# Kernel tuning notes

Hardware: AMD Instinct MI355X
Metric: run time of the kernel (lower is better)

The kernel has to match this reference:

```python
import jax, jax.numpy as jnp
import numpy as np

B, T, C, H = 4, 4096, 512, 64  # batch, seq(patches), n_embed, head_size

def setup_inputs() -> dict:
    key = jax.random.key(0)
    kx, kk, kq, kv = jax.random.split(key, 4)
    x = jax.random.normal(kx, (B, T, C), dtype=jnp.float32)
    # torch nn.Linear(n_embed, head_size).weight is [H, C]; store transposed [C, H]
    Wk = jax.random.normal(kk, (C, H), dtype=jnp.float32) / np.sqrt(C)
    Wq = jax.random.normal(kq, (C, H), dtype=jnp.float32) / np.sqrt(C)
    Wv = jax.random.normal(kv, (C, H), dtype=jnp.float32) / np.sqrt(C)
    return {"x": x, "Wk": Wk, "Wq": Wq, "Wv": Wv}

def reference(x, Wk, Wq, Wv):
    Bn, Tn, Cn = x.shape
    k = x @ Wk  # [B,T,H]
    q = x @ Wq
    v = x @ Wv
    # NOTE: original scales by C**-0.5 with C = n_embed (input dim), not head_size
    scores = jnp.einsum('bth,bsh->bts', q, k) * (Cn ** -0.5)  # [B,T,T]
    causal = jnp.tril(jnp.ones((Tn, Tn), dtype=bool))
    scores = jnp.where(causal, scores, -jnp.inf)
    attn = jax.nn.softmax(scores, axis=-1)
    return jnp.einsum('bts,bsh->bth', attn, v)  # [B,T,H]
```

## Files before the change

### kernel.cpp

```cpp
#include <hip/hip_runtime.h>
#include <hip/hip_bf16.h>

#define Bb 4
#define Tt 4096

typedef __bf16 bf16;
typedef __attribute__((ext_vector_type(8))) __bf16 bf16x8;
typedef __attribute__((ext_vector_type(4))) __bf16 bf16x4;
typedef __attribute__((ext_vector_type(2))) __bf16 bf16x2;
typedef __attribute__((ext_vector_type(4))) float f32x4;
typedef __attribute__((ext_vector_type(2))) unsigned int u32x2;
typedef __attribute__((ext_vector_type(4))) unsigned int u32x4;


__global__ __launch_bounds__(256) void wt_kernel(const float* __restrict__ Wk,
                                                 const float* __restrict__ Wq,
                                                 const float* __restrict__ Wv,
                                                 bf16* __restrict__ wt) {
  int idx = blockIdx.x * 256 + threadIdx.x;
  int mat = idx >> 15;
  int rem = idx & 32767;
  int n = rem >> 9;
  int k = rem & 511;
  const float* W = (mat == 0) ? Wk : (mat == 1) ? Wq : Wv;
  float v = W[k * 64 + n];
  if (mat == 1) v *= 0.0637587165f;
  wt[idx] = (bf16)v;
}

__global__ __launch_bounds__(256) void proj_kernel(const float* __restrict__ x,
                                                   const bf16* __restrict__ wt,
                                                   bf16* __restrict__ Kb,
                                                   bf16* __restrict__ Qb,
                                                   bf16* __restrict__ VTb) {
  __shared__ __attribute__((aligned(16))) bf16 xs[16][520];
  int tid = threadIdx.x;
  int row0 = blockIdx.x * 16;

  int sr = tid >> 4, sc = (tid & 15) * 4;
  const float* xr = x + (size_t)(row0 + sr) * 512;
#pragma unroll
  for (int j = 0; j < 8; ++j) {
    f32x4 a = *(const f32x4*)(xr + sc + j * 64);
    bf16x4 h;
#pragma unroll
    for (int e = 0; e < 4; ++e) h[e] = (bf16)a[e];
    *(bf16x4*)&xs[sr][sc + j * 64] = h;
  }
  __syncthreads();

  int wave = tid >> 6, lane = tid & 63, m = lane & 15, quad = lane >> 4;
  f32x4 acc[3];
#pragma unroll
  for (int i = 0; i < 3; ++i) acc[i] = (f32x4){0.f, 0.f, 0.f, 0.f};

#pragma unroll 4
  for (int kk = 0; kk < 512; kk += 32) {
    bf16x8 af = *(const bf16x8*)&xs[m][kk + quad * 8];
#pragma unroll
    for (int i = 0; i < 3; ++i) {
      int nt = wave * 3 + i;
      bf16x8 bfr = *(const bf16x8*)(wt + (nt >> 2) * 32768 +
                                    (((nt & 3) * 16) + m) * 512 + kk + quad * 8);
      acc[i] = __builtin_amdgcn_mfma_f32_16x16x32_bf16(af, bfr, acc[i], 0, 0, 0);
    }
  }

  int b = row0 >> 12, tloc = row0 & 4095;
#pragma unroll
  for (int i = 0; i < 3; ++i) {
    int nt = wave * 3 + i, mat = nt >> 2, n0 = (nt & 3) * 16;
    if (mat == 2) {
      bf16x4 pv;
#pragma unroll
      for (int r = 0; r < 4; ++r) pv[r] = (bf16)acc[i][r];
      *(bf16x4*)&VTb[((size_t)b * 64 + n0 + m) * 4096 + tloc + quad * 4] = pv;
    } else {
      bf16* dst = (mat == 0) ? Kb : Qb;
#pragma unroll
      for (int r = 0; r < 4; ++r)
        dst[(size_t)(row0 + quad * 4 + r) * 64 + n0 + m] = (bf16)acc[i][r];
    }
  }
}

static __device__ inline unsigned pk2(float lo, float hi) {
  bf16x2 t;
  t[0] = (bf16)lo;
  t[1] = (bf16)hi;
  return __builtin_bit_cast(unsigned int, t);
}
static __device__ inline void plswap(unsigned& a, unsigned& b) {
  u32x2 r = __builtin_amdgcn_permlane16_swap(a, b, false, false);
  a = r.x;
  b = r.y;
}

__global__ __launch_bounds__(256, 3) void attn_kernel(const bf16* __restrict__ Qb,
                                                      const bf16* __restrict__ Kb,
                                                      const bf16* __restrict__ VTb,
                                                      bf16* __restrict__ Opart,
                                                      float* __restrict__ Lpart,
                                                      float* __restrict__ out) {
  __shared__ __attribute__((aligned(16))) bf16 Kt[2][64][72];
  __shared__ __attribute__((aligned(16))) bf16 Vt[2][64][72];

  int tid = threadIdx.x, wave = tid >> 6, lane = tid & 63;
  int m = lane & 15, quad = lane >> 4, kq = quad * 8;

  int uu = 575 - (int)blockIdx.x;
  int b = uu / 144, u2 = uu % 144;
  int g = 0;
  while (u2 >= 2 * (g + 1) * (g + 2)) ++g;
  int rr = u2 - 2 * g * (g + 1);
  int qi2 = 4 * g + rr / (g + 1);
  int c = rr % (g + 1);
  int t0 = qi2 * 128;
  int s_beg = c * 512;
  int s_end = min(s_beg + 512, t0 + 128);
  int niter = (s_end - s_beg) >> 6;

  const bf16* Qp = Qb + ((size_t)b * Tt + t0 + wave * 16 + m) * 64;
  bf16x8 aq00 = *(const bf16x8*)(Qp + kq);
  bf16x8 aq01 = *(const bf16x8*)(Qp + 32 + kq);
  bf16x8 aq10 = *(const bf16x8*)(Qp + 4096 + kq);
  bf16x8 aq11 = *(const bf16x8*)(Qp + 4096 + 32 + kq);

  bf16x8 onesb;
#pragma unroll
  for (int j = 0; j < 8; ++j) onesb[j] = (bf16)1.0f;

  f32x4 o0[4], o1[4];
#pragma unroll
  for (int i = 0; i < 4; ++i) {
    o0[i] = (f32x4){0.f, 0.f, 0.f, 0.f};
    o1[i] = (f32x4){0.f, 0.f, 0.f, 0.f};
  }
  f32x4 lsum0 = (f32x4){0.f, 0.f, 0.f, 0.f};
  f32x4 lsum1 = (f32x4){0.f, 0.f, 0.f, 0.f};

  int r_ = tid >> 2, seg = tid & 3;
  const bf16* Kbase = Kb + (size_t)b * Tt * 64;
  const bf16* VTbase = VTb + (size_t)b * 64 * 4096;

  {
    const bf16* ks = Kbase + (size_t)(s_beg + r_) * 64 + seg * 16;
    bf16x8 k0 = *(const bf16x8*)ks;
    bf16x8 k1 = *(const bf16x8*)(ks + 8);
    const bf16* vs = VTbase + (size_t)r_ * 4096 + s_beg + seg * 16;
    bf16x8 v0 = *(const bf16x8*)vs;
    bf16x8 v1 = *(const bf16x8*)(vs + 8);
    *(bf16x8*)&Kt[0][r_][seg * 16] = k0;
    *(bf16x8*)&Kt[0][r_][seg * 16 + 8] = k1;
    *(bf16x8*)&Vt[0][r_][seg * 16] = v0;
    *(bf16x8*)&Vt[0][r_][seg * 16 + 8] = v1;
  }
  __syncthreads();

  int qrow0 = t0 + wave * 16 + m;

  for (int i = 0; i < niter; ++i) {
    int kv0 = s_beg + i * 64;
    int cb = i & 1;
    bool more = (i + 1 < niter);

    bf16x8 k0, k1, v0, v1;
    if (more) {
      int sn = kv0 + 64;
      const bf16* ks2 = Kbase + (size_t)(sn + r_) * 64 + seg * 16;
      k0 = *(const bf16x8*)ks2;
      k1 = *(const bf16x8*)(ks2 + 8);
      const bf16* vs2 = VTbase + (size_t)r_ * 4096 + sn + seg * 16;
      v0 = *(const bf16x8*)vs2;
      v1 = *(const bf16x8*)(vs2 + 8);
    }

    f32x4 s0[4], s1[4];
#pragma unroll
    for (int nt = 0; nt < 4; ++nt) {
      bf16x8 ak0 = *(const bf16x8*)&Kt[cb][nt * 16 + m][kq];
      bf16x8 ak1 = *(const bf16x8*)&Kt[cb][nt * 16 + m][32 + kq];
      f32x4 sa = (f32x4){0.f, 0.f, 0.f, 0.f};
      sa = __builtin_amdgcn_mfma_f32_16x16x32_bf16(ak0, aq00, sa, 0, 0, 0);
      sa = __builtin_amdgcn_mfma_f32_16x16x32_bf16(ak1, aq01, sa, 0, 0, 0);
      s0[nt] = sa;
      f32x4 sb = (f32x4){0.f, 0.f, 0.f, 0.f};
      sb = __builtin_amdgcn_mfma_f32_16x16x32_bf16(ak0, aq10, sb, 0, 0, 0);
      sb = __builtin_amdgcn_mfma_f32_16x16x32_bf16(ak1, aq11, sb, 0, 0, 0);
      s1[nt] = sb;
    }

    if (kv0 + 64 > t0) {
      int kvb = kv0 + 4 * quad;
#pragma unroll
      for (int nt = 0; nt < 4; ++nt)
#pragma unroll
        for (int r = 0; r < 4; ++r)
          if (kvb + nt * 16 + r > qrow0) s0[nt][r] = -1e30f;
    }
    if (kv0 >= t0 + 64) {
      int kvb = kv0 + 4 * quad;
#pragma unroll
      for (int nt = 0; nt < 4; ++nt)
#pragma unroll
        for (int r = 0; r < 4; ++r)
          if (kvb + nt * 16 + r > qrow0 + 64) s1[nt][r] = -1e30f;
    }

    unsigned pA0[4], pB0[4], pA1[4], pB1[4];
#pragma unroll
    for (int nt = 0; nt < 4; ++nt) {
      pA0[nt] = pk2(__builtin_amdgcn_exp2f(s0[nt][0]), __builtin_amdgcn_exp2f(s0[nt][1]));
      pB0[nt] = pk2(__builtin_amdgcn_exp2f(s0[nt][2]), __builtin_amdgcn_exp2f(s0[nt][3]));
      pA1[nt] = pk2(__builtin_amdgcn_exp2f(s1[nt][0]), __builtin_amdgcn_exp2f(s1[nt][1]));
      pB1[nt] = pk2(__builtin_amdgcn_exp2f(s1[nt][2]), __builtin_amdgcn_exp2f(s1[nt][3]));
    }

#pragma unroll
    for (int ch = 0; ch < 2; ++ch) {
      unsigned a0 = pA0[2 * ch], a1 = pA0[2 * ch + 1];
      unsigned c0 = pB0[2 * ch], c1 = pB0[2 * ch + 1];
      plswap(a0, a1);
      plswap(c0, c1);
      u32x4 ua0 = {a0, c0, a1, c1};
      bf16x8 ap0 = __builtin_bit_cast(bf16x8, ua0);
      lsum0 = __builtin_amdgcn_mfma_f32_16x16x32_bf16(ap0, onesb, lsum0, 0, 0, 0);

      int fb8 = (4 * ch + 2 * (quad & 1) + (quad >> 1)) * 8;
      bf16x8 bv[4];
#pragma unroll
      for (int nt = 0; nt < 4; ++nt)
        bv[nt] = *(const bf16x8*)&Vt[cb][nt * 16 + m][fb8];
#pragma unroll
      for (int nt = 0; nt < 4; ++nt)
        o0[nt] = __builtin_amdgcn_mfma_f32_16x16x32_bf16(ap0, bv[nt], o0[nt], 0, 0, 0);

      unsigned b0 = pA1[2 * ch], b1 = pA1[2 * ch + 1];
      unsigned d0 = pB1[2 * ch], d1 = pB1[2 * ch + 1];
      plswap(b0, b1);
      plswap(d0, d1);
      u32x4 ua1 = {b0, d0, b1, d1};
      bf16x8 ap1 = __builtin_bit_cast(bf16x8, ua1);
      lsum1 = __builtin_amdgcn_mfma_f32_16x16x32_bf16(ap1, onesb, lsum1, 0, 0, 0);
#pragma unroll
      for (int nt = 0; nt < 4; ++nt)
        o1[nt] = __builtin_amdgcn_mfma_f32_16x16x32_bf16(ap1, bv[nt], o1[nt], 0, 0, 0);
    }

    if (more) {
      int nb = cb ^ 1;
      *(bf16x8*)&Kt[nb][r_][seg * 16] = k0;
      *(bf16x8*)&Kt[nb][r_][seg * 16 + 8] = k1;
      *(bf16x8*)&Vt[nb][r_][seg * 16] = v0;
      *(bf16x8*)&Vt[nb][r_][seg * 16 + 8] = v1;
      __syncthreads();
    }
  }

  int rl0 = wave * 16 + quad * 4;
  if (g == 0) {
    float* op = out + ((size_t)b * Tt + t0) * 64;
#pragma unroll
    for (int r = 0; r < 4; ++r) {
      float inv0 = 1.0f / lsum0[r];
      float inv1 = 1.0f / lsum1[r];
#pragma unroll
      for (int nt = 0; nt < 4; ++nt) {
        op[(size_t)(rl0 + r) * 64 + nt * 16 + m] = o0[nt][r] * inv0;
        op[(size_t)(64 + rl0 + r) * 64 + nt * 16 + m] = o1[nt][r] * inv1;
      }
    }
  } else {
    int p = b * 140 + u2 - 4;
    bf16* Op = Opart + (size_t)p * 8192;
#pragma unroll
    for (int r = 0; r < 4; ++r)
#pragma unroll
      for (int nt = 0; nt < 4; ++nt) {
        Op[(rl0 + r) * 64 + nt * 16 + m] = (bf16)o0[nt][r];
        Op[(64 + rl0 + r) * 64 + nt * 16 + m] = (bf16)o1[nt][r];
      }
    if (m == 0) {
#pragma unroll
      for (int r = 0; r < 4; ++r) {
        Lpart[p * 128 + rl0 + r] = lsum0[r];
        Lpart[p * 128 + 64 + rl0 + r] = lsum1[r];
      }
    }
  }
}

__global__ __launch_bounds__(256) void combine_kernel(const bf16* __restrict__ Opart,
                                                      const float* __restrict__ Lpart,
                                                      float* __restrict__ out) {
  int blk = blockIdx.x;
  int b = blk / 224, rem = blk % 224;
  int qi2 = 4 + (rem >> 3), rq = rem & 7;
  int g = qi2 >> 2, nc = g + 1;
  int u2b = 2 * g * (g + 1) + (qi2 - 4 * g) * (g + 1);
  int pb = b * 140 + u2b - 4;
  int t = threadIdx.x, col = t & 63, rl = t >> 6;
#pragma unroll
  for (int rr = 0; rr < 4; ++rr) {
    int row128 = rq * 16 + rl * 4 + rr;
    float L = 0.f, acc = 0.f;
    for (int cc = 0; cc < nc; ++cc) {
      L += Lpart[(pb + cc) * 128 + row128];
      acc += (float)Opart[(size_t)(pb + cc) * 8192 + row128 * 64 + col];
    }
    out[((size_t)b * Tt + qi2 * 128 + row128) * 64 + col] = acc / L;
  }
}

extern "C" void kernel_launch(void* const* d_in, const int* in_sizes, int n_in,
                              void* d_out, int out_size, void* d_ws, size_t ws_size,
                              hipStream_t stream) {
  const float* x = (const float*)d_in[0];
  const float* Wk = (const float*)d_in[1];
  const float* Wq = (const float*)d_in[2];
  const float* Wv = (const float*)d_in[3];
  float* out = (float*)d_out;

  char* w = (char*)d_ws;
  bf16* wt = (bf16*)w;
  bf16* Kb = (bf16*)(w + 196608);
  bf16* Qb = (bf16*)(w + 2293760);
  bf16* VTb = (bf16*)(w + 4390912);
  bf16* Opart = (bf16*)(w + 6488064);
  float* Lpart = (float*)(w + 15925248);

  wt_kernel<<<384, 256, 0, stream>>>(Wk, Wq, Wv, wt);
  proj_kernel<<<1024, 256, 0, stream>>>(x, wt, Kb, Qb, VTb);
  attn_kernel<<<576, 256, 0, stream>>>(Qb, Kb, VTb, Opart, Lpart, out);
  combine_kernel<<<896, 256, 0, stream>>>(Opart, Lpart, out);
}
```

Before: 131.7 us.

## Fuse split-KV combine into attention via atomic counters; widen projection tiles

Removes the separate combine kernel. Each attention block now bumps a per-(batch, query-tile) atomic counter, and the last block to arrive reduces the partial outputs and row sums into the final result. The counters are zeroed in the weight-transpose kernel. The projection kernel now handles 32 rows per block instead of 16, so each weight fragment load feeds two MFMAs. s_setprio is also raised around the MFMA sections of the attention loop. Together these cut a kernel launch and its tail, at the cost of a serialized reduction tail in the last-arriving blocks plus threadfence overhead.

Measured after the change: 269.2 us. 104% more time.

```diff
diff --git a/kernel.cpp b/kernel.cpp
--- a/kernel.cpp
+++ b/kernel.cpp
@@ -16,7 +16,9 @@
 __global__ __launch_bounds__(256) void wt_kernel(const float* __restrict__ Wk,
                                                  const float* __restrict__ Wq,
                                                  const float* __restrict__ Wv,
-                                                 bf16* __restrict__ wt) {
+                                                 bf16* __restrict__ wt,
+                                                 int* __restrict__ cnt) {
+  if (blockIdx.x == 0 && threadIdx.x < 128) cnt[threadIdx.x] = 0;
   int idx = blockIdx.x * 256 + threadIdx.x;
   int mat = idx >> 15;
   int rem = idx & 32767;
@@ -33,53 +35,63 @@
                                                    bf16* __restrict__ Kb,
                                                    bf16* __restrict__ Qb,
                                                    bf16* __restrict__ VTb) {
-  __shared__ __attribute__((aligned(16))) bf16 xs[16][520];
+  __shared__ __attribute__((aligned(16))) bf16 xs[32][520];
   int tid = threadIdx.x;
-  int row0 = blockIdx.x * 16;
+  int row0 = blockIdx.x * 32;
 
   int sr = tid >> 4, sc = (tid & 15) * 4;
-  const float* xr = x + (size_t)(row0 + sr) * 512;
-#pragma unroll
-  for (int j = 0; j < 8; ++j) {
-    f32x4 a = *(const f32x4*)(xr + sc + j * 64);
-    bf16x4 h;
-#pragma unroll
-    for (int e = 0; e < 4; ++e) h[e] = (bf16)a[e];
-    *(bf16x4*)&xs[sr][sc + j * 64] = h;
+#pragma unroll
+  for (int s = 0; s < 2; ++s) {
+    const float* xr = x + (size_t)(row0 + s * 16 + sr) * 512;
+#pragma unroll
+    for (int j = 0; j < 8; ++j) {
+      f32x4 a = *(const f32x4*)(xr + sc + j * 64);
+      bf16x4 h;
+#pragma unroll
+      for (int e = 0; e < 4; ++e) h[e] = (bf16)a[e];
+      *(bf16x4*)&xs[s * 16 + sr][sc + j * 64] = h;
+    }
   }
   __syncthreads();
 
   int wave = tid >> 6, lane = tid & 63, m = lane & 15, quad = lane >> 4;
-  f32x4 acc[3];
-#pragma unroll
-  for (int i = 0; i < 3; ++i) acc[i] = (f32x4){0.f, 0.f, 0.f, 0.f};
+  f32x4 acc[2][3];
+#pragma unroll
+  for (int s = 0; s < 2; ++s)
+#pragma unroll
+    for (int i = 0; i < 3; ++i) acc[s][i] = (f32x4){0.f, 0.f, 0.f, 0.f};
 
 #pragma unroll 4
   for (int kk = 0; kk < 512; kk += 32) {
-    bf16x8 af = *(const bf16x8*)&xs[m][kk + quad * 8];
+    bf16x8 af0 = *(const bf16x8*)&xs[m][kk + quad * 8];
+    bf16x8 af1 = *(const bf16x8*)&xs[16 + m][kk + quad * 8];
 #pragma unroll
     for (int i = 0; i < 3; ++i) {
       int nt = wave * 3 + i;
       bf16x8 bfr = *(const bf16x8*)(wt + (nt >> 2) * 32768 +
                                     (((nt & 3) * 16) + m) * 512 + kk + quad * 8);
-      acc[i] = __builtin_amdgcn_mfma_f32_16x16x32_bf16(af, bfr, acc[i], 0, 0, 0);
+      acc[0][i] = __builtin_amdgcn_mfma_f32_16x16x32_bf16(af0, bfr, acc[0][i], 0, 0, 0);
+      acc[1][i] = __builtin_amdgcn_mfma_f32_16x16x32_bf16(af1, bfr, acc[1][i], 0, 0, 0);
     }
   }
 
   int b = row0 >> 12, tloc = row0 & 4095;
 #pragma unroll
-  for (int i = 0; i < 3; ++i) {
-    int nt = wave * 3 + i, mat = nt >> 2, n0 = (nt & 3) * 16;
-    if (mat == 2) {
-      bf16x4 pv;
-#pragma unroll
-      for (int r = 0; r < 4; ++r) pv[r] = (bf16)acc[i][r];
-      *(bf16x4*)&VTb[((size_t)b * 64 + n0 + m) * 4096 + tloc + quad * 4] = pv;
-    } else {
-      bf16* dst = (mat == 0) ? Kb : Qb;
-#pragma unroll
-      for (int r = 0; r < 4; ++r)
-        dst[(size_t)(row0 + quad * 4 + r) * 64 + n0 + m] = (bf16)acc[i][r];
+  for (int s = 0; s < 2; ++s) {
+#pragma unroll
+    for (int i = 0; i < 3; ++i) {
+      int nt = wave * 3 + i, mat = nt >> 2, n0 = (nt & 3) * 16;
+      if (mat == 2) {
+        bf16x4 pv;
+#pragma unroll
+        for (int r = 0; r < 4; ++r) pv[r] = (bf16)acc[s][i][r];
+        *(bf16x4*)&VTb[((size_t)b * 64 + n0 + m) * 4096 + tloc + s * 16 + quad * 4] = pv;
+      } else {
+        bf16* dst = (mat == 0) ? Kb : Qb;
+#pragma unroll
+        for (int r = 0; r < 4; ++r)
+          dst[(size_t)(row0 + s * 16 + quad * 4 + r) * 64 + n0 + m] = (bf16)acc[s][i][r];
+      }
     }
   }
 }
@@ -101,9 +113,11 @@
                                                       const bf16* __restrict__ VTb,
                                                       bf16* __restrict__ Opart,
                                                       float* __restrict__ Lpart,
+                                                      int* __restrict__ cnt,
                                                       float* __restrict__ out) {
   __shared__ __attribute__((aligned(16))) bf16 Kt[2][64][72];
   __shared__ __attribute__((aligned(16))) bf16 Vt[2][64][72];
+  __shared__ int lastf;
 
   int tid = threadIdx.x, wave = tid >> 6, lane = tid & 63;
   int m = lane & 15, quad = lane >> 4, kq = quad * 8;
@@ -176,6 +190,7 @@
     }
 
     f32x4 s0[4], s1[4];
+    __builtin_amdgcn_s_setprio(1);
 #pragma unroll
     for (int nt = 0; nt < 4; ++nt) {
       bf16x8 ak0 = *(const bf16x8*)&Kt[cb][nt * 16 + m][kq];
@@ -189,6 +204,7 @@
       sb = __builtin_amdgcn_mfma_f32_16x16x32_bf16(ak1, aq11, sb, 0, 0, 0);
       s1[nt] = sb;
     }
+    __builtin_amdgcn_s_setprio(0);
 
     if (kv0 + 64 > t0) {
       int kvb = kv0 + 4 * quad;
@@ -216,6 +232,7 @@
       pB1[nt] = pk2(__builtin_amdgcn_exp2f(s1[nt][2]), __builtin_amdgcn_exp2f(s1[nt][3]));
     }
 
+    __builtin_amdgcn_s_setprio(1);
 #pragma unroll
     for (int ch = 0; ch < 2; ++ch) {
       unsigned a0 = pA0[2 * ch], a1 = pA0[2 * ch + 1];
@@ -246,6 +263,7 @@
       for (int nt = 0; nt < 4; ++nt)
         o1[nt] = __builtin_amdgcn_mfma_f32_16x16x32_bf16(ap1, bv[nt], o1[nt], 0, 0, 0);
     }
+    __builtin_amdgcn_s_setprio(0);
 
     if (more) {
       int nb = cb ^ 1;
@@ -287,28 +305,27 @@
         Lpart[p * 128 + 64 + rl0 + r] = lsum1[r];
       }
     }
-  }
-}
-
-__global__ __launch_bounds__(256) void combine_kernel(const bf16* __restrict__ Opart,
-                                                      const float* __restrict__ Lpart,
-                                                      float* __restrict__ out) {
-  int blk = blockIdx.x;
-  int b = blk / 224, rem = blk % 224;
-  int qi2 = 4 + (rem >> 3), rq = rem & 7;
-  int g = qi2 >> 2, nc = g + 1;
-  int u2b = 2 * g * (g + 1) + (qi2 - 4 * g) * (g + 1);
-  int pb = b * 140 + u2b - 4;
-  int t = threadIdx.x, col = t & 63, rl = t >> 6;
-#pragma unroll
-  for (int rr = 0; rr < 4; ++rr) {
-    int row128 = rq * 16 + rl * 4 + rr;
-    float L = 0.f, acc = 0.f;
-    for (int cc = 0; cc < nc; ++cc) {
-      L += Lpart[(pb + cc) * 128 + row128];
-      acc += (float)Opart[(size_t)(pb + cc) * 8192 + row128 * 64 + col];
-    }
-    out[((size_t)b * Tt + qi2 * 128 + row128) * 64 + col] = acc / L;
+    __threadfence();
+    __syncthreads();
+    if (tid == 0) {
+      int old = atomicAdd(&cnt[b * 32 + qi2], 1);
+      lastf = (old == g);
+    }
+    __syncthreads();
+    if (lastf) {
+      __threadfence();
+      int nc = g + 1;
+      int pb = b * 140 + 2 * g * (g + 1) + (qi2 - 4 * g) * (g + 1) - 4;
+      int col = tid & 63, rl = tid >> 6;
+      for (int row = rl; row < 128; row += 4) {
+        float L = 0.f, acc = 0.f;
+        for (int cc = 0; cc < nc; ++cc) {
+          L += Lpart[(pb + cc) * 128 + row];
+          acc += (float)Opart[(size_t)(pb + cc) * 8192 + row * 64 + col];
+        }
+        out[((size_t)b * Tt + t0 + row) * 64 + col] = acc / L;
+      }
+    }
   }
 }
 
@@ -328,9 +345,9 @@
   bf16* VTb = (bf16*)(w + 4390912);
   bf16* Opart = (bf16*)(w + 6488064);
   float* Lpart = (float*)(w + 15925248);
-
-  wt_kernel<<<384, 256, 0, stream>>>(Wk, Wq, Wv, wt);
-  proj_kernel<<<1024, 256, 0, stream>>>(x, wt, Kb, Qb, VTb);
-  attn_kernel<<<576, 256, 0, stream>>>(Qb, Kb, VTb, Opart, Lpart, out);
-  combine_kernel<<<896, 256, 0, stream>>>(Opart, Lpart, out);
-}
+  int* cnt = (int*)(w + 16211968);
+
+  wt_kernel<<<384, 256, 0, stream>>>(Wk, Wq, Wv, wt, cnt);
+  proj_kernel<<<512, 256, 0, stream>>>(x, wt, Kb, Qb, VTb);
+  attn_kernel<<<576, 256, 0, stream>>>(Qb, Kb, VTb, Opart, Lpart, cnt, out);
+}
```
